# Performance work log

Measured on AMD Instinct MI355X. Metric: run time of the kernel, lower is better.

The kernel has to match this reference:

```python
import jax, jax.numpy as jnp
import numpy as np

QUERY_LEVELS = jnp.array([300, 500, 900, 1500], dtype=jnp.int32)
MAX_K = 1500
NUM_BOUNDARIES = 3
MAX_OBJECTS = 1500
SCALE = MAX_OBJECTS / NUM_BOUNDARIES * 0.3  # 150.0


def _layernorm(x, g, b, eps=1e-5):
    m = jnp.mean(x, axis=-1, keepdims=True)
    v = jnp.var(x, axis=-1, keepdims=True)
    return (x - m) * jax.lax.rsqrt(v + eps) * g + b


def setup_inputs() -> dict:
    key = jax.random.key(0)
    ks = jax.random.split(key, 14)
    B, C, H, W = 8, 256, 100, 100
    s = 0.02
    return {
        "density_feature": jax.random.normal(ks[0], (B, C, H, W), jnp.float32),
        "encoder_features": jax.random.normal(ks[1], (B, C, H, W), jnp.float32),
        # input_norm (LayerNorm over 2*C)
        "ln_in_g": jnp.ones((2 * C,), jnp.float32),
        "ln_in_b": jnp.zeros((2 * C,), jnp.float32),
        # fc_boundary: Linear(2C->C), Linear(C->3)
        "fcb_w1": jax.random.normal(ks[2], (C, 2 * C), jnp.float32) * s,
        "fcb_b1": jnp.zeros((C,), jnp.float32),
        "fcb_w2": jax.random.normal(ks[3], (NUM_BOUNDARIES, C), jnp.float32) * s,
        "fcb_b2": jnp.full((NUM_BOUNDARIES,), -3.0, jnp.float32),
        "cr_ln_g": jnp.ones((C,), jnp.float32),
        "cr_ln_b": jnp.zeros((C,), jnp.float32),
        "cr_w1": jax.random.normal(ks[4], (C, C), jnp.float32) * s,
        "cr_b1": jnp.zeros((C,), jnp.float32),
        "cr_w2": jax.random.normal(ks[5], (1, C), jnp.float32) * s,
        "cr_b2": jnp.full((1,), 4.0, jnp.float32),
        # channel attention 1x1 convs: C->C//16->C
        "ca_w1": jax.random.normal(ks[6], (C // 16, C), jnp.float32) * s,
        "ca_b1": jnp.zeros((C // 16,), jnp.float32),
        "ca_w2": jax.random.normal(ks[7], (C, C // 16), jnp.float32) * s,
        "ca_b2": jnp.zeros((C,), jnp.float32),
        # spatial attention 7x7 conv, 2->1, no bias
        "sa_w": jax.random.normal(ks[8], (1, 2, 7, 7), jnp.float32) * s,
        # spatial_weight_conv 1x1, C->1
        "sw_w": jax.random.normal(ks[9], (1, C), jnp.float32) * s,
        "sw_b": jnp.zeros((1,), jnp.float32),
    }


def reference(density_feature, encoder_features, ln_in_g, ln_in_b,
              fcb_w1, fcb_b1, fcb_w2, fcb_b2,
              cr_ln_g, cr_ln_b, cr_w1, cr_b1, cr_w2, cr_b2,
              ca_w1, ca_b1, ca_w2, ca_b2, sa_w, sw_w, sw_b):
    B, C, H, W = density_feature.shape
    df = jnp.clip(density_feature, -5.0, 5.0)
    ef = jnp.clip(encoder_features, -5.0, 5.0)

    # ---- boundary prediction from density feature ----
    feat_avg = jnp.mean(df, axis=(2, 3))            # [B, C]
    feat_max = jnp.max(df, axis=(2, 3))             # [B, C]
    gfeat = jnp.concatenate([feat_avg, feat_max], axis=1)  # [B, 2C]
    gfeat = _layernorm(gfeat, ln_in_g, ln_in_b)
    h = jax.nn.relu(gfeat @ fcb_w1.T + fcb_b1)
    raw_boundaries = h @ fcb_w2.T + fcb_b2           # [B, 3]
    # cumulative: b_i = sum_{j<=i} (softplus(raw_j)*SCALE + 5)
    boundaries = jnp.cumsum(jax.nn.softplus(raw_boundaries) * SCALE + 5.0, axis=1)

    cr = _layernorm(feat_avg, cr_ln_g, cr_ln_b)
    cr = jax.nn.relu(cr @ cr_w1.T + cr_b1)
    pred_count = jax.nn.softplus(cr @ cr_w2.T + cr_b2)[:, 0]  # [B]

    # ---- num_queries via boundary comparison (eval: N_eval = pred_count) ----
    level = ((pred_count > boundaries[:, 0]).astype(jnp.int32)
             + (pred_count > boundaries[:, 1]).astype(jnp.int32)
             + (pred_count > boundaries[:, 2]).astype(jnp.int32))
    num_queries = QUERY_LEVELS[level]

    # ---- CBAM channel attention ----
    x = ef
    gap = jnp.mean(x, axis=(2, 3))                   # [B, C]
    ca = jax.nn.relu(gap @ ca_w1.T + ca_b1)
    ca = jax.nn.sigmoid(ca @ ca_w2.T + ca_b2)        # [B, C]
    x = x * ca[:, :, None, None]

    # ---- CBAM spatial attention ----
    sa_avg = jnp.mean(x, axis=1, keepdims=True)      # [B,1,H,W]
    sa_max = jnp.max(x, axis=1, keepdims=True)
    sa = jnp.concatenate([sa_avg, sa_max], axis=1)   # [B,2,H,W]
    sa = jax.lax.conv_general_dilated(sa, sa_w, (1, 1), [(3, 3), (3, 3)],
                                      dimension_numbers=("NCHW", "OIHW", "NCHW"))
    x = x * jax.nn.sigmoid(sa)

    # ---- spatial weight map + topk reference points ----
    wmap = jax.nn.sigmoid(jnp.einsum("bchw,oc->bohw", x, sw_w) + sw_b[None, :, None, None])
    spatial_weight_map = wmap.reshape(B, 1, H * W)
    weight_flat = wmap.reshape(B, H * W)
    actual_k = min(H * W, MAX_K)
    _, topk_ind = jax.lax.top_k(weight_flat, actual_k)   # [B, k]
    topk_y = ((topk_ind // W).astype(jnp.float32) + 0.5) / H
    topk_x = ((topk_ind % W).astype(jnp.float32) + 0.5) / W
    ref_points = jnp.stack([topk_x, topk_y], axis=-1)    # [B,k,2]
    ref_points = jnp.concatenate([ref_points, jnp.full_like(ref_points, 0.05)], axis=-1)
    if actual_k < MAX_K:
        pad = jnp.zeros((B, MAX_K - actual_k, 4), ref_points.dtype)
        ref_points = jnp.concatenate([ref_points, pad], axis=1)

    return (boundaries, raw_boundaries, pred_count, num_queries,
            spatial_weight_map, ref_points)
```

## Files before the change

kernel.cpp:

```cpp
#include <hip/hip_runtime.h>
#include <cstdint>
#include <cstddef>

#define BB 8
#define CC 256
#define HH 100
#define WW 100
#define HW 10000
#define KTOP 1500
#define QB 64

#define WS_AVG   0
#define WS_MAX   2048
#define WS_GAP   4096
#define WS_CA    6144
#define WS_CASW  8192
#define WS_SW    10240
#define WS_SAVG  90240
#define WS_SMAX  170240
#define WS_SEL   250240
#define WS_AK    250248

#define O_BND 0
#define O_RAW 24
#define O_CNT 48
#define O_NQ  56
#define O_WMAP 64
#define O_REF 80064

__device__ __forceinline__ float clip5(float v){ return fminf(fmaxf(v, -5.f), 5.f); }
__device__ __forceinline__ float softplusf(float x){ return fmaxf(x, 0.f) + log1pf(expf(-fabsf(x))); }
__device__ __forceinline__ float sigmoidf(float x){ return 1.f / (1.f + expf(-x)); }

__device__ __forceinline__ float wsum(float v){
#pragma unroll
  for (int o = 32; o; o >>= 1) v += __shfl_down(v, o, 64);
  return v;
}
__device__ __forceinline__ float wmaxr(float v){
#pragma unroll
  for (int o = 32; o; o >>= 1) v = fmaxf(v, __shfl_down(v, o, 64));
  return v;
}

__device__ __forceinline__ float bsum256(float v, volatile float* red){
  v = wsum(v);
  int w = threadIdx.x >> 6;
  if ((threadIdx.x & 63) == 0) red[w] = v;
  __syncthreads();
  float r = (red[0] + red[1]) + (red[2] + red[3]);
  __syncthreads();
  return r;
}

__global__ __launch_bounds__(256) void k_reduce(const float* __restrict__ df,
                                                const float* __restrict__ ef,
                                                float* __restrict__ ws){
  int blk = blockIdx.x;
  bool isDf = blk < 2048;
  int bc = isDf ? blk : blk - 2048;
  const float4* __restrict__ src =
      reinterpret_cast<const float4*>((isDf ? df : ef) + (size_t)bc * HW);
  int t = threadIdx.x;
  float4 v[10];
#pragma unroll
  for (int k = 0; k < 10; k++){
    int idx = t + 256 * k;
    v[k] = src[idx < 2500 ? idx : (idx - 2500)];
  }
  __builtin_amdgcn_sched_barrier(0);

  float s = 0.f, m = -1e30f;
#pragma unroll
  for (int k = 0; k < 9; k++){
    float a = clip5(v[k].x), b = clip5(v[k].y), c = clip5(v[k].z), d = clip5(v[k].w);
    s += (a + b) + (c + d);
    m = fmaxf(m, fmaxf(fmaxf(a, b), fmaxf(c, d)));
  }
  if (t < (2500 - 9 * 256)){
    float a = clip5(v[9].x), b = clip5(v[9].y), c = clip5(v[9].z), d = clip5(v[9].w);
    s += (a + b) + (c + d);
    m = fmaxf(m, fmaxf(fmaxf(a, b), fmaxf(c, d)));
  }

  __shared__ float rs[4], rm[4];
  s = wsum(s); m = wmaxr(m);
  int w = t >> 6;
  if ((t & 63) == 0){ rs[w] = s; rm[w] = m; }
  __syncthreads();
  if (t == 0){
    float S = (rs[0] + rs[1]) + (rs[2] + rs[3]);
    float M = fmaxf(fmaxf(rm[0], rm[1]), fmaxf(rm[2], rm[3]));
    if (isDf){ ws[WS_AVG + bc] = S * (1.f / HW); ws[WS_MAX + bc] = M; }
    else      { ws[WS_GAP + bc] = S * (1.f / HW); }
  }
}

__global__ __launch_bounds__(256) void k_head(float* __restrict__ ws,
    const float* __restrict__ ln_g, const float* __restrict__ ln_b,
    const float* __restrict__ fw1, const float* __restrict__ fb1,
    const float* __restrict__ fw2, const float* __restrict__ fb2,
    const float* __restrict__ crg, const float* __restrict__ crb,
    const float* __restrict__ cw1, const float* __restrict__ cb1,
    const float* __restrict__ cw2, const float* __restrict__ cb2,
    const float* __restrict__ caw1, const float* __restrict__ cab1,
    const float* __restrict__ caw2, const float* __restrict__ cab2,
    const float* __restrict__ sw_w, float* __restrict__ out){
  int b = blockIdx.x, t = threadIdx.x;
  __shared__ float red[4];
  __shared__ __align__(16) float gl[512];
  __shared__ __align__(16) float hl[256];
  __shared__ float rawl[3];
  __shared__ float bnd[3];
  __shared__ __align__(16) float al[16];

  float fa = ws[WS_AVG + b * CC + t];
  float fm = ws[WS_MAX + b * CC + t];

  float s  = bsum256(fa + fm, red);
  float s2 = bsum256(fa * fa + fm * fm, red);
  float mean = s * (1.f / 512.f);
  float var  = s2 * (1.f / 512.f) - mean * mean;
  float inv  = rsqrtf(var + 1e-5f);
  gl[t]       = (fa - mean) * inv * ln_g[t]       + ln_b[t];
  gl[t + 256] = (fm - mean) * inv * ln_g[t + 256] + ln_b[t + 256];
  __syncthreads();

  {
    const float4* __restrict__ glv = reinterpret_cast<const float4*>(gl);
    const float4* __restrict__ w1v = reinterpret_cast<const float4*>(fw1 + t * 512);
    float acc = fb1[t];
#pragma unroll 8
    for (int k = 0; k < 128; k++){
      float4 g = glv[k], w = w1v[k];
      acc += g.x * w.x + g.y * w.y + g.z * w.z + g.w * w.w;
    }
    hl[t] = fmaxf(acc, 0.f);
  }
  __syncthreads();
  if (t < 3){
    const float4* __restrict__ hv  = reinterpret_cast<const float4*>(hl);
    const float4* __restrict__ w2v = reinterpret_cast<const float4*>(fw2 + t * 256);
    float r = fb2[t];
#pragma unroll 8
    for (int k = 0; k < 64; k++){
      float4 h = hv[k], w = w2v[k];
      r += h.x * w.x + h.y * w.y + h.z * w.z + h.w * w.w;
    }
    rawl[t] = r;
  }
  __syncthreads();
  if (t == 0){
    float cum = 0.f;
    for (int o = 0; o < 3; o++){
      float rv = rawl[o];
      out[O_RAW + b * 3 + o] = rv;
      cum += softplusf(rv) * 150.f + 5.f;
      out[O_BND + b * 3 + o] = cum;
      bnd[o] = cum;
    }
  }
  __syncthreads();

  float sc  = bsum256(fa, red);
  float sc2 = bsum256(fa * fa, red);
  float m2 = sc * (1.f / 256.f);
  float v2 = sc2 * (1.f / 256.f) - m2 * m2;
  float inv2 = rsqrtf(v2 + 1e-5f);
  hl[t] = (fa - m2) * inv2 * crg[t] + crb[t];
  __syncthreads();
  float h2;
  {
    const float4* __restrict__ hv  = reinterpret_cast<const float4*>(hl);
    const float4* __restrict__ w1v = reinterpret_cast<const float4*>(cw1 + t * 256);
    float acc2 = cb1[t];
#pragma unroll 8
    for (int k = 0; k < 64; k++){
      float4 h = hv[k], w = w1v[k];
      acc2 += h.x * w.x + h.y * w.y + h.z * w.z + h.w * w.w;
    }
    h2 = fmaxf(acc2, 0.f);
  }
  float pv = bsum256(h2 * cw2[t], red);
  if (t == 0){
    float pred = softplusf(pv + cb2[0]);
    out[O_CNT + b] = pred;
    int lvl = (pred > bnd[0]) + (pred > bnd[1]) + (pred > bnd[2]);
    const float QL[4] = {300.f, 500.f, 900.f, 1500.f};
    out[O_NQ + b] = QL[lvl];
  }

  float gp = ws[WS_GAP + b * CC + t];
  __syncthreads();
  hl[t] = gp;
  __syncthreads();
  if (t < 16){
    const float4* __restrict__ hv  = reinterpret_cast<const float4*>(hl);
    const float4* __restrict__ w1v = reinterpret_cast<const float4*>(caw1 + t * 256);
    float a = cab1[t];
#pragma unroll 8
    for (int k = 0; k < 64; k++){
      float4 h = hv[k], w = w1v[k];
      a += h.x * w.x + h.y * w.y + h.z * w.z + h.w * w.w;
    }
    al[t] = fmaxf(a, 0.f);
  }
  __syncthreads();
  float a2 = cab2[t];
  {
    const float4* __restrict__ av  = reinterpret_cast<const float4*>(al);
    const float4* __restrict__ w2v = reinterpret_cast<const float4*>(caw2 + t * 16);
#pragma unroll
    for (int k = 0; k < 4; k++){
      float4 h = av[k], w = w2v[k];
      a2 += h.x * w.x + h.y * w.y + h.z * w.z + h.w * w.w;
    }
  }
  float cav = sigmoidf(a2);
  ws[WS_CA + b * CC + t]   = cav;
  ws[WS_CASW + b * CC + t] = cav * sw_w[t];
}

__device__ __forceinline__ void px_acc(const float4& v, float ca, float cs,
                                       float4& sum, float4& mx, float4& sw){
  float a = clip5(v.x), b = clip5(v.y), c = clip5(v.z), d = clip5(v.w);
  sum.x += a * ca; sum.y += b * ca; sum.z += c * ca; sum.w += d * ca;
  mx.x = fmaxf(mx.x, a * ca); mx.y = fmaxf(mx.y, b * ca);
  mx.z = fmaxf(mx.z, c * ca); mx.w = fmaxf(mx.w, d * ca);
  sw.x = fmaf(a, cs, sw.x); sw.y = fmaf(b, cs, sw.y);
  sw.z = fmaf(c, cs, sw.z); sw.w = fmaf(d, cs, sw.w);
}

__global__ __launch_bounds__(256) void k_pixel(const float* __restrict__ ef,
                                               float* __restrict__ ws){
  int b = blockIdx.y;
  int t = threadIdx.x;
  int w = t >> 6, lane = t & 63;
  __shared__ float caL[256], cswL[256];
  __shared__ float4 part[3][4][QB];
  caL[t]  = ws[WS_CA + b * CC + t];
  cswL[t] = ws[WS_CASW + b * CC + t];
  __syncthreads();

  int q = blockIdx.x * QB + lane;
  const size_t st = HW / 4;
  size_t off = (q < (int)st) ? (size_t)q : 0;
  const float4* __restrict__ base =
      reinterpret_cast<const float4*>(ef + (size_t)b * CC * HW) + off;
  int c0 = w * 64;

  float4 sum = {0.f, 0.f, 0.f, 0.f};
  float4 mx  = {-1e30f, -1e30f, -1e30f, -1e30f};
  float4 sw  = {0.f, 0.f, 0.f, 0.f};

  float4 A[8], Bv[8];
#pragma unroll
  for (int j = 0; j < 8; j++) A[j] = base[(size_t)(c0 + j) * st];
#pragma unroll
  for (int s = 0; s < 4; s++){
    int cA = c0 + (2 * s) * 8;
    int cB = c0 + (2 * s + 1) * 8;
#pragma unroll
    for (int j = 0; j < 8; j++) Bv[j] = base[(size_t)(cB + j) * st];
#pragma unroll
    for (int j = 0; j < 8; j++) px_acc(A[j], caL[cA + j], cswL[cA + j], sum, mx, sw);
    if (s < 3){
      int cN = c0 + (2 * s + 2) * 8;
#pragma unroll
      for (int j = 0; j < 8; j++) A[j] = base[(size_t)(cN + j) * st];
    }
#pragma unroll
    for (int j = 0; j < 8; j++) px_acc(Bv[j], caL[cB + j], cswL[cB + j], sum, mx, sw);
  }

  part[0][w][lane] = sum;
  part[1][w][lane] = mx;
  part[2][w][lane] = sw;
  __syncthreads();
  if (t < QB){
    float4 S = part[0][0][t], M = part[1][0][t], W4 = part[2][0][t];
#pragma unroll
    for (int wv = 1; wv < 4; wv++){
      float4 s1 = part[0][wv][t], m1 = part[1][wv][t], w1 = part[2][wv][t];
      S.x += s1.x; S.y += s1.y; S.z += s1.z; S.w += s1.w;
      M.x = fmaxf(M.x, m1.x); M.y = fmaxf(M.y, m1.y);
      M.z = fmaxf(M.z, m1.z); M.w = fmaxf(M.w, m1.w);
      W4.x += w1.x; W4.y += w1.y; W4.z += w1.z; W4.w += w1.w;
    }
    int q2 = blockIdx.x * QB + t;
    if (q2 < (int)st){
      float4 avg = {S.x * (1.f / 256.f), S.y * (1.f / 256.f),
                    S.z * (1.f / 256.f), S.w * (1.f / 256.f)};
      reinterpret_cast<float4*>(ws + WS_SAVG + (size_t)b * HW)[q2] = avg;
      reinterpret_cast<float4*>(ws + WS_SMAX + (size_t)b * HW)[q2] = M;
      reinterpret_cast<float4*>(ws + WS_SW   + (size_t)b * HW)[q2] = W4;
    }
  }
}

__global__ __launch_bounds__(256) void k_conv(const float* __restrict__ ws,
                                              const float* __restrict__ sa_w,
                                              const float* __restrict__ sw_b,
                                              float* __restrict__ out){
  __shared__ float wc[98];
  if (threadIdx.x < 98) wc[threadIdx.x] = sa_w[threadIdx.x];
  __syncthreads();
  int b = blockIdx.y;
  int p = blockIdx.x * 256 + threadIdx.x;
  if (p >= HW) return;
  int h = p / WW, w = p - h * WW;
  const float* s0 = ws + WS_SAVG + (size_t)b * HW;
  const float* s1 = ws + WS_SMAX + (size_t)b * HW;
  float acc = 0.f;
#pragma unroll
  for (int kh = 0; kh < 7; kh++){
    int hy = h + kh - 3;
    if (hy < 0 || hy >= HH) continue;
#pragma unroll
    for (int kw = 0; kw < 7; kw++){
      int wx = w + kw - 3;
      if (wx < 0 || wx >= WW) continue;
      int q = hy * WW + wx;
      acc += s0[q] * wc[kh * 7 + kw] + s1[q] * wc[49 + kh * 7 + kw];
    }
  }
  float wm = sigmoidf(ws[WS_SW + (size_t)b * HW + p] * sigmoidf(acc) + sw_b[0]);
  out[O_WMAP + (size_t)b * HW + p] = wm;
}

__global__ __launch_bounds__(1024) void k_select(const float* __restrict__ outw,
                                                 float* __restrict__ ws,
                                                 float* __restrict__ out){
  __shared__ unsigned long long red64[16];
  __shared__ unsigned red32[16];
  __shared__ unsigned slo, shi, sbc;
  __shared__ unsigned acnt, runbase;
  int b = blockIdx.x, t = threadIdx.x;
  int w = t >> 6, lane = t & 63;

  const float* src = outw + O_WMAP + (size_t)b * HW;
  unsigned rv[10];
#pragma unroll
  for (int j = 0; j < 10; j++){
    int i = t + j * 1024;
    rv[j] = (i < HW) ? __float_as_uint(src[i]) : 0u;
  }

  unsigned lo = 0u, hi = 0xFFFFFFFFu;
  while (lo < hi){
    unsigned span = hi - lo;
    unsigned q1 = lo + (span >> 2);
    unsigned q2 = lo + (span >> 1);
    unsigned q3 = lo + span - (span >> 2);
    unsigned long long pk = 0;
#pragma unroll
    for (int j = 0; j < 10; j++){
      unsigned v = rv[j];
      pk += (unsigned long long)(v > q1)
          + ((unsigned long long)(v > q2) << 16)
          + ((unsigned long long)(v > q3) << 32);
    }
#pragma unroll
    for (int o = 32; o; o >>= 1) pk += __shfl_down(pk, o, 64);
    if (lane == 0) red64[w] = pk;
    __syncthreads();
    if (t == 0){
      unsigned long long tot = 0;
#pragma unroll
      for (int q = 0; q < 16; q++) tot += red64[q];
      unsigned c1 = (unsigned)(tot & 0xFFFFu);
      unsigned c2 = (unsigned)((tot >> 16) & 0xFFFFu);
      unsigned c3 = (unsigned)((tot >> 32) & 0xFFFFu);
      unsigned nlo, nhi;
      if (c1 < (unsigned)KTOP)      { nlo = lo;      nhi = q1; }
      else if (c2 < (unsigned)KTOP) { nlo = q1 + 1u; nhi = q2; }
      else if (c3 < (unsigned)KTOP) { nlo = q2 + 1u; nhi = q3; }
      else                          { nlo = q3 + 1u; nhi = hi; }
      slo = nlo; shi = nhi;
    }
    __syncthreads();
    lo = slo; hi = shi;
    __syncthreads();
  }
  unsigned vthr = lo;

  {
    unsigned c = 0;
#pragma unroll
    for (int j = 0; j < 10; j++) c += (rv[j] > vthr) ? 1u : 0u;
#pragma unroll
    for (int o = 32; o; o >>= 1) c += __shfl_down((int)c, o, 64);
    if (lane == 0) red32[w] = c;
    __syncthreads();
    if (t == 0){
      unsigned tot = 0;
#pragma unroll
      for (int q = 0; q < 16; q++) tot += red32[q];
      sbc = tot;
      acnt = 0; runbase = 0;
    }
    __syncthreads();
  }
  unsigned nabove = sbc;
  int neq = KTOP - (int)nabove;
  if (t == 0) reinterpret_cast<int*>(ws)[WS_SEL + b] = (int)nabove;

  unsigned long long* AK = reinterpret_cast<unsigned long long*>(ws + WS_AK) + (size_t)b * KTOP;
#pragma unroll
  for (int j = 0; j < 10; j++){
    int i = t + j * 1024;
    bool p = (i < HW) && (rv[j] > vthr);
    unsigned long long m = __ballot(p);
    unsigned base = 0;
    if (lane == 0 && m) base = atomicAdd(&acnt, (unsigned)__popcll(m));
    base = (unsigned)__shfl((int)base, 0, 64);
    if (p){
      unsigned pos = base + (unsigned)__popcll(m & ((1ull << lane) - 1ull));
      AK[pos] = ((unsigned long long)rv[j] << 32) | (unsigned long long)(0xFFFFFFFFu - (unsigned)i);
    }
  }

  for (int j = 0; j < 10; j++){
    int i = j * 1024 + t;
    bool eq = (i < HW) && (rv[j] == vthr);
    unsigned long long bal = __ballot(eq);
    if (lane == 0) red32[w] = (unsigned)__popcll(bal);
    __syncthreads();
    unsigned pre = runbase;
    for (int q = 0; q < w; q++) pre += red32[q];
    unsigned myr = pre + (unsigned)__popcll(bal & ((1ull << lane) - 1ull));
    if (eq && myr < (unsigned)neq){
      int pos = (int)nabove + (int)myr;
      float y = ((float)(i / WW) + 0.5f) * (1.f / HH);
      float x = ((float)(i % WW) + 0.5f) * (1.f / WW);
      float* rp = out + O_REF + ((size_t)b * KTOP + pos) * 4;
      rp[0] = x; rp[1] = y; rp[2] = 0.05f; rp[3] = 0.05f;
    }
    __syncthreads();
    if (t == 0){
      unsigned tot = 0;
#pragma unroll
      for (int q = 0; q < 16; q++) tot += red32[q];
      runbase += tot;
    }
    __syncthreads();
    if (runbase >= (unsigned)neq) break;
  }
}

__global__ __launch_bounds__(128) void k_rank(const float* __restrict__ ws,
                                              float* __restrict__ out){
  int b = blockIdx.x, chunk = blockIdx.y, t = threadIdx.x;
  int nA = reinterpret_cast<const int*>(ws)[WS_SEL + b];
  __shared__ unsigned long long K[KTOP];
  const unsigned long long* AK =
      reinterpret_cast<const unsigned long long*>(ws + WS_AK) + (size_t)b * KTOP;
  for (int i = t; i < nA; i += 128) K[i] = AK[i];
  __syncthreads();
  int i = chunk * 128 + t;
  if (i >= nA) return;
  unsigned long long Ki = K[i];
  int r = 0;
  for (int j = 0; j < nA; j++) r += (K[j] > Ki);
  unsigned idx = 0xFFFFFFFFu - (unsigned)(Ki & 0xFFFFFFFFull);
  float y = ((float)(idx / WW) + 0.5f) * (1.f / HH);
  float x = ((float)(idx % WW) + 0.5f) * (1.f / WW);
  float* rp = out + O_REF + ((size_t)b * KTOP + r) * 4;
  rp[0] = x; rp[1] = y; rp[2] = 0.05f; rp[3] = 0.05f;
}

extern "C" void kernel_launch(void* const* d_in, const int* in_sizes, int n_in,
                              void* d_out, int out_size, void* d_ws, size_t ws_size,
                              hipStream_t stream) {
  const float* df   = (const float*)d_in[0];
  const float* ef   = (const float*)d_in[1];
  const float* ln_g = (const float*)d_in[2];
  const float* ln_b = (const float*)d_in[3];
  const float* fw1  = (const float*)d_in[4];
  const float* fb1  = (const float*)d_in[5];
  const float* fw2  = (const float*)d_in[6];
  const float* fb2  = (const float*)d_in[7];
  const float* crg  = (const float*)d_in[8];
  const float* crb  = (const float*)d_in[9];
  const float* cw1  = (const float*)d_in[10];
  const float* cb1  = (const float*)d_in[11];
  const float* cw2  = (const float*)d_in[12];
  const float* cb2  = (const float*)d_in[13];
  const float* caw1 = (const float*)d_in[14];
  const float* cab1 = (const float*)d_in[15];
  const float* caw2 = (const float*)d_in[16];
  const float* cab2 = (const float*)d_in[17];
  const float* sa_w = (const float*)d_in[18];
  const float* sw_w = (const float*)d_in[19];
  const float* sw_b = (const float*)d_in[20];
  float* out = (float*)d_out;
  float* ws  = (float*)d_ws;

  k_reduce<<<4096, 256, 0, stream>>>(df, ef, ws);
  k_head<<<8, 256, 0, stream>>>(ws, ln_g, ln_b, fw1, fb1, fw2, fb2,
                                crg, crb, cw1, cb1, cw2, cb2,
                                caw1, cab1, caw2, cab2, sw_w, out);
  k_pixel<<<dim3(40, 8), 256, 0, stream>>>(ef, ws);
  k_conv<<<dim3(40, 8), 256, 0, stream>>>(ws, sa_w, sw_b, out);
  k_select<<<8, 1024, 0, stream>>>(out, ws, out);
  k_rank<<<dim3(8, 12), 128, 0, stream>>>(ws, out);
}
```

Baseline: 146.7 us.

## Reduce each channel plane with one wavefront using double-buffered loads

The channel reduction kernel now gives each 64-lane wavefront a whole (batch, channel) plane instead of a whole 256-thread block, so the cross-wave shared-memory reduction and barrier go away. Each wave streams the plane through two 8-deep float4 register buffers, issuing the next batch of loads before reducing the current one to keep memory requests in flight. The grid shrinks to a quarter as many blocks. Each wave now has a longer serial chain of loads, so the change relies on enough waves being resident to keep HBM busy.

```diff
diff --git a/kernel.cpp b/kernel.cpp
--- a/kernel.cpp
+++ b/kernel.cpp
@@ -53,46 +53,52 @@
   return r;
 }
 
+__device__ __forceinline__ void acc1(const float4& v, float& s, float& m){
+  float a = clip5(v.x), b = clip5(v.y), c = clip5(v.z), d = clip5(v.w);
+  s += (a + b) + (c + d);
+  m = fmaxf(m, fmaxf(fmaxf(a, b), fmaxf(c, d)));
+}
+
 __global__ __launch_bounds__(256) void k_reduce(const float* __restrict__ df,
                                                 const float* __restrict__ ef,
                                                 float* __restrict__ ws){
-  int blk = blockIdx.x;
-  bool isDf = blk < 2048;
-  int bc = isDf ? blk : blk - 2048;
+  int gw = blockIdx.x * 4 + (threadIdx.x >> 6);
+  bool isDf = gw < 2048;
+  int bc = isDf ? gw : gw - 2048;
+  int lane = threadIdx.x & 63;
   const float4* __restrict__ src =
       reinterpret_cast<const float4*>((isDf ? df : ef) + (size_t)bc * HW);
-  int t = threadIdx.x;
-  float4 v[10];
-#pragma unroll
-  for (int k = 0; k < 10; k++){
-    int idx = t + 256 * k;
-    v[k] = src[idx < 2500 ? idx : (idx - 2500)];
-  }
-  __builtin_amdgcn_sched_barrier(0);
 
   float s = 0.f, m = -1e30f;
-#pragma unroll
-  for (int k = 0; k < 9; k++){
-    float a = clip5(v[k].x), b = clip5(v[k].y), c = clip5(v[k].z), d = clip5(v[k].w);
-    s += (a + b) + (c + d);
-    m = fmaxf(m, fmaxf(fmaxf(a, b), fmaxf(c, d)));
-  }
-  if (t < (2500 - 9 * 256)){
-    float a = clip5(v[9].x), b = clip5(v[9].y), c = clip5(v[9].z), d = clip5(v[9].w);
-    s += (a + b) + (c + d);
-    m = fmaxf(m, fmaxf(fmaxf(a, b), fmaxf(c, d)));
-  }
-
-  __shared__ float rs[4], rm[4];
+  float4 A[8], Bv[8];
+
+#pragma unroll
+  for (int j = 0; j < 8; j++) A[j]  = src[64 * j + lane];
+#pragma unroll
+  for (int j = 0; j < 8; j++) Bv[j] = src[512 + 64 * j + lane];
+#pragma unroll
+  for (int j = 0; j < 8; j++) acc1(A[j], s, m);
+#pragma unroll
+  for (int j = 0; j < 8; j++) A[j]  = src[1024 + 64 * j + lane];
+#pragma unroll
+  for (int j = 0; j < 8; j++) acc1(Bv[j], s, m);
+#pragma unroll
+  for (int j = 0; j < 8; j++) Bv[j] = src[1536 + 64 * j + lane];
+#pragma unroll
+  for (int j = 0; j < 8; j++) acc1(A[j], s, m);
+#pragma unroll
+  for (int j = 0; j < 7; j++) A[j]  = src[2048 + 64 * j + lane];
+  A[7] = src[(2496 + lane < 2500) ? (2496 + lane) : lane];
+#pragma unroll
+  for (int j = 0; j < 8; j++) acc1(Bv[j], s, m);
+#pragma unroll
+  for (int j = 0; j < 7; j++) acc1(A[j], s, m);
+  if (lane < 4) acc1(A[7], s, m);
+
   s = wsum(s); m = wmaxr(m);
-  int w = t >> 6;
-  if ((t & 63) == 0){ rs[w] = s; rm[w] = m; }
-  __syncthreads();
-  if (t == 0){
-    float S = (rs[0] + rs[1]) + (rs[2] + rs[3]);
-    float M = fmaxf(fmaxf(rm[0], rm[1]), fmaxf(rm[2], rm[3]));
-    if (isDf){ ws[WS_AVG + bc] = S * (1.f / HW); ws[WS_MAX + bc] = M; }
-    else      { ws[WS_GAP + bc] = S * (1.f / HW); }
+  if (lane == 0){
+    if (isDf){ ws[WS_AVG + bc] = s * (1.f / HW); ws[WS_MAX + bc] = m; }
+    else      { ws[WS_GAP + bc] = s * (1.f / HW); }
   }
 }
 
@@ -496,7 +502,7 @@
   float* out = (float*)d_out;
   float* ws  = (float*)d_ws;
 
-  k_reduce<<<4096, 256, 0, stream>>>(df, ef, ws);
+  k_reduce<<<1024, 256, 0, stream>>>(df, ef, ws);
   k_head<<<8, 256, 0, stream>>>(ws, ln_g, ln_b, fw1, fb1, fw2, fb2,
                                 crg, crb, cw1, cb1, cw2, cb2,
                                 caw1, cab1, caw2, cab2, sw_w, out);
```

Measured after the change: 146.7 us. About the same (+0.0%).
